# Optimization experiments

Measured on AMD Instinct MI355X. Metric: run time of the kernel, lower is better.

Reference implementation:

```python
import jax, jax.numpy as jnp
import numpy as np

# dims: batch, input channels, hidden neurons, actions, time bins
B, C_IN, HID, OUT, T = 1024, 8, 300, 2, 300
TS, TAU_SR, THETA = 1.0, 10.0, 10.0   # simulation step, SRM kernel tau, spike threshold
TAU_REF, SCALE_REF = 2.0, 2.0          # refractory alpha-kernel tau and scale
TAU_RHO, SCALE_RHO = 1.0, 1.0          # surrogate-gradient pdf params (SLAYER)
K = 100                                 # SRM kernel truncation length (alpha kernel is negligible past 10*tau)

_t = np.arange(K, dtype=np.float32) * TS
SRM = jnp.asarray((_t / TAU_SR) * np.exp(1.0 - _t / TAU_SR))  # alpha PSP kernel, eps(0)=0


def psp(x):
    # slayer.psp: causal temporal convolution of the weighted input with the SRM alpha kernel. x: [B, C, T]
    b, c, t = x.shape
    lhs = x.reshape(b * c, 1, t)
    rhs = SRM[::-1].reshape(1, 1, K).astype(x.dtype)  # flip so correlation == causal convolution
    out = jax.lax.conv_general_dilated(lhs, rhs, (1,), [(K - 1, 0)],
                                       dimension_numbers=('NCH', 'OIH', 'NCH'))
    return out.reshape(b, c, t)


@jax.custom_vjp
def heaviside(u):
    # forward: hard threshold; backward: SLAYER surrogate pdf scaleRho/tauRho * exp(-|u|/tauRho)
    return (u >= 0).astype(u.dtype)

def _hs_fwd(u):
    return heaviside(u), u

def _hs_bwd(u, g):
    return (g * (SCALE_RHO / TAU_RHO) * jnp.exp(-jnp.abs(u) / TAU_RHO),)

heaviside.defvjp(_hs_fwd, _hs_bwd)


def spike(u):
    # slayer.spike: integrate-and-fire with an alpha-shaped refractory response
    # refKernel(n) = -scaleRef*theta * (n*Ts/tauRef) * exp(1 - n*Ts/tauRef)
    # realized exactly via a 2-state linear recurrence (x = n*a^n term, y = a^n term)
    a = jnp.exp(jnp.asarray(-TS / TAU_REF, u.dtype))
    A = jnp.asarray(-SCALE_REF * THETA * np.e * TS / TAU_REF, u.dtype)

    def step(carry, u_t):
        x, y = carry                     # x: accumulated refractory potential at this step
        s = heaviside(u_t + x - THETA)   # membrane (psp + refractory) vs threshold
        y2 = y + A * s                   # spike injects impulse into the alpha-kernel state
        return (a * (x + y2), a * y2), s

    u_tbc = jnp.moveaxis(u, -1, 0)  # [T, B, C]
    z = jnp.zeros(u.shape[:-1], u.dtype)
    _, s = jax.lax.scan(step, (z, z), u_tbc)
    return jnp.moveaxis(s, 0, -1)


def setup_inputs():
    key = jax.random.key(0)
    k1, k2, k3 = jax.random.split(key, 3)
    # CartPoleEncoder output is a spike train: Bernoulli(0.3) spikes over T bins
    encoded_input = (jax.random.uniform(k1, (B, C_IN, T)) < 0.3).astype(jnp.float32)
    W1 = jax.random.normal(k2, (HID, C_IN), dtype=jnp.float32)
    W2 = jax.random.normal(k3, (OUT, HID), dtype=jnp.float32)
    return {"encoded_input": encoded_input, "W1": W1, "W2": W2}


def reference(encoded_input, W1, W2):
    # fc is a 1x1x1 conv3d == per-timestep dense layer over channels
    sl1 = spike(psp(jnp.einsum('bit,oi->bot', encoded_input, W1)))  # [B, 300, T]
    sl2 = spike(psp(jnp.einsum('bht,oh->bot', sl1, W2)))            # [B, 2, T]
    logits = jnp.sum(sl2, axis=-1)                                   # spike counts -> Categorical logits [B, 2]
    g = jax.random.gumbel(jax.random.key(42), logits.shape, logits.dtype)
    pi = jnp.argmax(logits + g, axis=-1)                             # Categorical sample via Gumbel-max
    logp = jax.nn.log_softmax(logits, axis=-1)
    logp_pi = jnp.take_along_axis(logp, pi[:, None], axis=-1)[:, 0]
    return logits, pi, logp_pi
```

## Files before the change

kernel.cpp:

```cpp
#include <hip/hip_runtime.h>
#include <stdint.h>


#define NB    1024
#define CIN   8
#define HID   300
#define TLEN  300
#define KTAP  99
#define THETA 10.0f

#define LDS_K1 134240

typedef double d2v __attribute__((ext_vector_type(2)));

__device__ __forceinline__ void threefry2x32(uint32_t c0, uint32_t c1,
                                             uint32_t& o0, uint32_t& o1) {
  const uint32_t k0 = 0u, k1 = 42u;
  const uint32_t k2 = k0 ^ k1 ^ 0x1BD11BDAu;
  uint32_t x0 = c0 + k0, x1 = c1 + k1;
#define TFR(r) { x0 += x1; x1 = (x1 << (r)) | (x1 >> (32 - (r))); x1 ^= x0; }
  TFR(13) TFR(15) TFR(26) TFR(6)  x0 += k1; x1 += k2 + 1u;
  TFR(17) TFR(29) TFR(16) TFR(24) x0 += k2; x1 += k0 + 2u;
  TFR(13) TFR(15) TFR(26) TFR(6)  x0 += k0; x1 += k1 + 3u;
  TFR(17) TFR(29) TFR(16) TFR(24) x0 += k1; x1 += k2 + 4u;
  TFR(13) TFR(15) TFR(26) TFR(6)  x0 += k2; x1 += k0 + 5u;
#undef TFR
  o0 = x0; o1 = x1;
}

__device__ __forceinline__ float jax_uniform_from_bits(uint32_t bits) {
  uint32_t fb = (bits >> 9) | 0x3F800000u;
  float f = __uint_as_float(fb) - 1.0f;
  const float tiny = 1.17549435e-38f;
  float u = __fadd_rn(f, tiny);
  return fmaxf(tiny, u);
}

__global__ void snn_taps_kernel(double* __restrict__ tapsG) {
  const int i = threadIdx.x;
  if (i < 107) {
    const int j = i - 2;
    double v = 0.0;
    if (j >= 1 && j <= KTAP) {
      float q  = (float)j / 10.0f;
      float ef = (float)exp((double)(1.0f - q));
      v = (double)__fmul_rn(q, ef);
    }
    tapsG[i] = v;
  }
}

__global__ __launch_bounds__(320)
void snn_enc_kernel(const float* __restrict__ enc, uint32_t* __restrict__ encBG) {
  const int b = blockIdx.x, t = threadIdx.x;
  if (t < TLEN) {
    uint32_t m = 0u;
#pragma unroll
    for (int c = 0; c < CIN; ++c)
      if (enc[b * (CIN * TLEN) + c * TLEN + t] != 0.0f) m |= (1u << c);
    encBG[b * TLEN + t] = m;
  }
}

__global__ __launch_bounds__(1024, 1)
void snn_l1_kernel(const float* __restrict__ W1,
                   const double* __restrict__ tapsG,
                   const uint32_t* __restrict__ encBG,
                   unsigned long long* __restrict__ maskG) {
  extern __shared__ char smem[];
  double* kL   = (double*)(smem);
  float*  xbuf = (float*)(smem + 864);
  float*  ubuf = (float*)(smem + 103520);

  const int tid  = threadIdx.x;
  const int lane = tid & 63;
  const int wv   = tid >> 6;
  const int bh   = blockIdx.x;
  const int b    = blockIdx.y;
  const int h    = bh * 64 + lane;

  if (tid < 107) kL[tid] = tapsG[tid];
  for (int i = tid; i < 101 * 64; i += 1024)
    xbuf[i] = 0.0f;
  __syncthreads();

  float w1f[8];
#pragma unroll
  for (int c = 0; c < 8; ++c)
    w1f[c] = (h < HID) ? W1[h * 8 + c] : 0.0f;

  for (int t = wv; t < TLEN; t += 16) {
    const uint32_t bits = encBG[__builtin_amdgcn_readfirstlane(b * TLEN + t)];
    float xf = 0.0f;
#pragma unroll
    for (int c = 0; c < 8; ++c) {
      float wsel = (bits & (1u << c)) ? w1f[c] : 0.0f;
      xf = __fadd_rn(xf, wsel);
    }
    xbuf[(101 + t) * 64 + lane] = xf;
  }
  __syncthreads();

  const float arf = (float)0.6065306597126334;
  const float Af  = (float)-27.182818284590452;

#define LOADGRP(g, xf_, kt_) do {                                         \
    const float* xg_ = xbuf + (96 + t0 - ((g) << 3)) * 64 + lane;         \
    _Pragma("unroll")                                                     \
    for (int u_ = 0; u_ < 8; ++u_) xf_[u_] = xg_[u_ * 64];                \
    const d2v* kp_ = (const d2v*)(kL + ((g) << 3));                       \
    _Pragma("unroll")                                                     \
    for (int u_ = 0; u_ < 5; ++u_) {                                      \
      d2v kv_ = kp_[u_];                                                  \
      kt_[2 * u_] = kv_.x; kt_[2 * u_ + 1] = kv_.y;                       \
    }                                                                     \
    kt_[10] = kL[((g) << 3) + 10];                                        \
  } while (0)

#define FMAGRP(xf_, kt_) do {                                             \
    _Pragma("unroll")                                                     \
    for (int d_ = 0; d_ < 8; ++d_) {                                      \
      const double xv_ = (double)xf_[7 - d_];                             \
      a0 += kt_[d_ + 0] * xv_;                                            \
      a1 += kt_[d_ + 1] * xv_;                                            \
      a2 += kt_[d_ + 2] * xv_;                                            \
      a3 += kt_[d_ + 3] * xv_;                                            \
    }                                                                     \
  } while (0)

  auto fir_chunk = [&](int s, int c, int bufsel) {
    const int t0 = 60 * s + 4 * c;
    double a0 = 0.0, a1 = 0.0, a2 = 0.0, a3 = 0.0;
    float  xfA[8], xfB[8];
    double ktA[11], ktB[11];
    LOADGRP(0, xfA, ktA);
#pragma clang loop unroll(disable)
    for (int g = 0; g < 12; g += 2) {
      LOADGRP(g + 1, xfB, ktB);
      FMAGRP(xfA, ktA);
      LOADGRP(g + 2, xfA, ktA);
      FMAGRP(xfB, ktB);
    }
    FMAGRP(xfA, ktA);
    float* ub = ubuf + bufsel * (60 * 64) + (4 * c) * 64 + lane;
    ub[0]   = (float)a0;
    ub[64]  = (float)a1;
    ub[128] = (float)a2;
    ub[192] = (float)a3;
  };

  float RX = 0.0f, RY = 0.0f;
  unsigned long long* maskW = maskG + (size_t)b * (5 * TLEN) + bh * TLEN;

  auto scan_stage = [&](int s) {
    const float* ub = ubuf + (s & 1) * (60 * 64) + lane;
#pragma clang loop unroll(disable)
    for (int r = 0; r < 60; r += 4) {
      float u0 = ub[(r + 0) * 64];
      float u1 = ub[(r + 1) * 64];
      float u2 = ub[(r + 2) * 64];
      float u3 = ub[(r + 3) * 64];
#pragma unroll
      for (int d = 0; d < 4; ++d) {
        float umem = (d == 0) ? u0 : (d == 1) ? u1 : (d == 2) ? u2 : u3;
        float v  = __fsub_rn(__fadd_rn(umem, RX), THETA);
        bool  sp = (v >= 0.0f) && (h < HID);
        unsigned long long bal = __ballot(sp);
        if (lane == 0) maskW[60 * s + r + d] = bal;
        float sf = sp ? 1.0f : 0.0f;
        float y2 = __fadd_rn(RY, __fmul_rn(Af, sf));
        RX = __fmul_rn(arf, __fadd_rn(RX, y2));
        RY = __fmul_rn(arf, y2);
      }
    }
  };

  if (wv < 15) fir_chunk(0, wv, 0);
  __syncthreads();
#pragma clang loop unroll(disable)
  for (int s = 0; s < 5; ++s) {
    if (wv == 0)      scan_stage(s);
    else if (s < 4)   fir_chunk(s + 1, wv - 1, (s + 1) & 1);
    __syncthreads();
  }
#undef LOADGRP
#undef FMAGRP
}

__global__ __launch_bounds__(320)
void snn_l2_kernel(const float* __restrict__ W2,
                   const unsigned long long* __restrict__ maskG,
                   float* __restrict__ out) {
  __shared__ double             kD[100];
  __shared__ double             W2D[2 * HID];
  __shared__ unsigned long long maskL[5 * TLEN];
  __shared__ double             zD[2 * 304];
  __shared__ float              u2L[2 * 304];
  __shared__ float              lgL[2];

  const int tid = threadIdx.x;
  const int b   = blockIdx.x;

  const float arf = (float)0.6065306597126334;
  const float Af  = (float)-27.182818284590452;

  for (int j = tid; j < 100; j += 320) {
    float q  = (float)j / 10.0f;
    float ef = (float)exp((double)(1.0f - q));
    kD[j] = (double)__fmul_rn(q, ef);
  }
  for (int i = tid; i < 2 * HID; i += 320)
    W2D[i] = (double)W2[i];
  for (int i = tid; i < 5 * TLEN; i += 320)
    maskL[i] = maskG[(size_t)b * (5 * TLEN) + i];
  __syncthreads();

  if (tid < TLEN) {
    const int t = tid;
    double z0 = 0.0, z1 = 0.0;
#pragma unroll
    for (int w5 = 0; w5 < 5; ++w5) {
      const unsigned long long mm = maskL[w5 * TLEN + t];
      const int kend = (w5 == 4) ? (HID - 256) : 64;
      for (int k = 0; k < kend; ++k) {
        const bool bit = (mm >> k) & 1ull;
        const int  hh  = w5 * 64 + k;
        z0 += bit ? W2D[hh] : 0.0;
        z1 += bit ? W2D[HID + hh] : 0.0;
      }
    }
    zD[t]       = (double)((float)z0);
    zD[304 + t] = (double)((float)z1);
  }
  __syncthreads();

  if (tid < TLEN) {
    const int t = tid;
    double a0 = 0.0, a1 = 0.0;
    const int jmax = (t < KTAP) ? t : KTAP;
    for (int j = 1; j <= jmax; ++j) {
      const double kk = kD[j];
      a0 += kk * zD[t - j];
      a1 += kk * zD[304 + t - j];
    }
    u2L[t]       = (float)a0;
    u2L[304 + t] = (float)a1;
  }
  __syncthreads();

  if (tid < 2) {
    float RX = 0.0f, RY = 0.0f;
    int cnt = 0;
    for (int t = 0; t < TLEN; ++t) {
      float u  = u2L[tid * 304 + t];
      float v  = __fsub_rn(__fadd_rn(u, RX), THETA);
      bool  sp = (v >= 0.0f);
      cnt += sp ? 1 : 0;
      float sf = sp ? 1.0f : 0.0f;
      float y2 = __fadd_rn(RY, __fmul_rn(Af, sf));
      RX = __fmul_rn(arf, __fadd_rn(RX, y2));
      RY = __fmul_rn(arf, y2);
    }
    lgL[tid] = (float)cnt;
  }
  __syncthreads();

  if (tid == 0) {
    float l0 = lgL[0], l1 = lgL[1];
    uint32_t o0, o1;
    threefry2x32(0u, 2u * (uint32_t)b, o0, o1);
    float g0 = -logf(-logf(jax_uniform_from_bits(o0 ^ o1)));
    threefry2x32(0u, 2u * (uint32_t)b + 1u, o0, o1);
    float g1 = -logf(-logf(jax_uniform_from_bits(o0 ^ o1)));

    float v0 = __fadd_rn(l0, g0);
    float v1 = __fadd_rn(l1, g1);
    int   pi = (v1 > v0) ? 1 : 0;
    float m   = fmaxf(l0, l1);
    float s0f = __fsub_rn(l0, m), s1f = __fsub_rn(l1, m);
    float lse = logf(__fadd_rn(expf(s0f), expf(s1f)));
    float lp  = __fsub_rn(pi ? s1f : s0f, lse);

    out[2 * b + 0] = l0;
    out[2 * b + 1] = l1;
    out[2048 + b]  = (float)pi;
    out[3072 + b]  = lp;
  }
}

extern "C" void kernel_launch(void* const* d_in, const int* in_sizes, int n_in,
                              void* d_out, int out_size, void* d_ws, size_t ws_size,
                              hipStream_t stream) {
  const float* enc = (const float*)d_in[0];
  const float* W1  = (const float*)d_in[1];
  const float* W2  = (const float*)d_in[2];
  float* out = (float*)d_out;

  double*             tapsG = (double*)d_ws;
  uint32_t*           encBG = (uint32_t*)((char*)d_ws + 1024);
  unsigned long long* maskG = (unsigned long long*)((char*)d_ws + 1024 + 1228800);

  hipFuncSetAttribute((const void*)snn_l1_kernel,
                      hipFuncAttributeMaxDynamicSharedMemorySize, LDS_K1);

  snn_taps_kernel<<<dim3(1), dim3(128), 0, stream>>>(tapsG);
  snn_enc_kernel<<<dim3(NB), dim3(320), 0, stream>>>(enc, encBG);
  snn_l1_kernel<<<dim3(5, NB), dim3(1024), LDS_K1, stream>>>(W1, tapsG, encBG, maskG);
  snn_l2_kernel<<<dim3(NB), dim3(320), 0, stream>>>(W2, maskG, out);
}
```

Measured before the change: 834.5 us.

## Pack layer-1 FIR inputs as float4 per lane and read taps via scalar loads

New measurement: 799.4 us. 4.2% less time.

```diff
diff --git a/kernel.cpp b/kernel.cpp
--- a/kernel.cpp
+++ b/kernel.cpp
@@ -9,9 +9,9 @@
 #define KTAP  99
 #define THETA 10.0f
 
-#define LDS_K1 134240
-
-typedef double d2v __attribute__((ext_vector_type(2)));
+#define LDS_K1 134144
+
+typedef float f4 __attribute__((ext_vector_type(4)));
 
 __device__ __forceinline__ void threefry2x32(uint32_t c0, uint32_t c1,
                                              uint32_t& o0, uint32_t& o1) {
@@ -68,9 +68,9 @@
                    const uint32_t* __restrict__ encBG,
                    unsigned long long* __restrict__ maskG) {
   extern __shared__ char smem[];
-  double* kL   = (double*)(smem);
-  float*  xbuf = (float*)(smem + 864);
-  float*  ubuf = (float*)(smem + 103520);
+  float* xq   = (float*)(smem);
+  f4*    xqv  = (f4*)(smem);
+  float* ubuf = (float*)(smem + 103424);
 
   const int tid  = threadIdx.x;
   const int lane = tid & 63;
@@ -79,9 +79,8 @@
   const int b    = blockIdx.y;
   const int h    = bh * 64 + lane;
 
-  if (tid < 107) kL[tid] = tapsG[tid];
   for (int i = tid; i < 101 * 64; i += 1024)
-    xbuf[i] = 0.0f;
+    xqv[i] = (f4)(0.0f);
   __syncthreads();
 
   float w1f[8];
@@ -97,51 +96,41 @@
       float wsel = (bits & (1u << c)) ? w1f[c] : 0.0f;
       xf = __fadd_rn(xf, wsel);
     }
-    xbuf[(101 + t) * 64 + lane] = xf;
+    const int slot = 101 + t;
+    xq[(slot >> 2) * 256 + lane * 4 + (slot & 3)] = xf;
   }
   __syncthreads();
 
   const float arf = (float)0.6065306597126334;
   const float Af  = (float)-27.182818284590452;
-
-#define LOADGRP(g, xf_, kt_) do {                                         \
-    const float* xg_ = xbuf + (96 + t0 - ((g) << 3)) * 64 + lane;         \
-    _Pragma("unroll")                                                     \
-    for (int u_ = 0; u_ < 8; ++u_) xf_[u_] = xg_[u_ * 64];                \
-    const d2v* kp_ = (const d2v*)(kL + ((g) << 3));                       \
-    _Pragma("unroll")                                                     \
-    for (int u_ = 0; u_ < 5; ++u_) {                                      \
-      d2v kv_ = kp_[u_];                                                  \
-      kt_[2 * u_] = kv_.x; kt_[2 * u_ + 1] = kv_.y;                       \
-    }                                                                     \
-    kt_[10] = kL[((g) << 3) + 10];                                        \
-  } while (0)
-
-#define FMAGRP(xf_, kt_) do {                                             \
-    _Pragma("unroll")                                                     \
-    for (int d_ = 0; d_ < 8; ++d_) {                                      \
-      const double xv_ = (double)xf_[7 - d_];                             \
-      a0 += kt_[d_ + 0] * xv_;                                            \
-      a1 += kt_[d_ + 1] * xv_;                                            \
-      a2 += kt_[d_ + 2] * xv_;                                            \
-      a3 += kt_[d_ + 3] * xv_;                                            \
-    }                                                                     \
-  } while (0)
 
   auto fir_chunk = [&](int s, int c, int bufsel) {
     const int t0 = 60 * s + 4 * c;
     double a0 = 0.0, a1 = 0.0, a2 = 0.0, a3 = 0.0;
-    float  xfA[8], xfB[8];
-    double ktA[11], ktB[11];
-    LOADGRP(0, xfA, ktA);
 #pragma clang loop unroll(disable)
-    for (int g = 0; g < 12; g += 2) {
-      LOADGRP(g + 1, xfB, ktB);
-      FMAGRP(xfA, ktA);
-      LOADGRP(g + 2, xfA, ktA);
-      FMAGRP(xfB, ktB);
-    }
-    FMAGRP(xfA, ktA);
+    for (int g = 0; g < 13; ++g) {
+      const int m0 = __builtin_amdgcn_readfirstlane(g << 3);
+      const int qb = (96 + t0 - (g << 3)) >> 2;
+      f4 v0 = xqv[qb * 64 + lane];
+      f4 v1 = xqv[(qb + 1) * 64 + lane];
+      double kt[11];
+#pragma unroll
+      for (int u = 0; u < 11; ++u) kt[u] = tapsG[m0 + u];
+      double x64[8];
+#pragma unroll
+      for (int u = 0; u < 4; ++u) {
+        x64[u]     = (double)v0[u];
+        x64[4 + u] = (double)v1[u];
+      }
+#pragma unroll
+      for (int d = 0; d < 8; ++d) {
+        const double xv = x64[7 - d];
+        a0 += kt[d + 0] * xv;
+        a1 += kt[d + 1] * xv;
+        a2 += kt[d + 2] * xv;
+        a3 += kt[d + 3] * xv;
+      }
+    }
     float* ub = ubuf + bufsel * (60 * 64) + (4 * c) * 64 + lane;
     ub[0]   = (float)a0;
     ub[64]  = (float)a1;
@@ -183,8 +172,6 @@
     else if (s < 4)   fir_chunk(s + 1, wv - 1, (s + 1) & 1);
     __syncthreads();
   }
-#undef LOADGRP
-#undef FMAGRP
 }
 
 __global__ __launch_bounds__(320)
```
